# Optimization experiments

Hardware: AMD Instinct MI355X
Metric: run time of the kernel (lower is better)

Reference implementation:

```python
import jax, jax.numpy as jnp
import numpy as np

N_NODES = 50000
N_EDGES = 1600000
GL = [512, 256, 16]
LL = [16, 16]


def setup_inputs() -> dict:
    key = jax.random.key(0)
    ks = jax.random.split(key, 10)
    H = jax.random.normal(ks[0], (N_NODES, GL[0]), dtype=jnp.float32)
    edge_index = jax.random.randint(ks[1], (2, N_EDGES), 0, N_NODES, dtype=jnp.int64)
    edge_vals = jax.random.uniform(ks[2], (N_EDGES,), dtype=jnp.float32)
    def uni(k, shape, fan_out):
        stdv = 1.0 / np.sqrt(fan_out)
        return jax.random.uniform(k, shape, minval=-stdv, maxval=stdv, dtype=jnp.float32)
    W1 = uni(ks[3], (GL[0], GL[1]), GL[1])
    b1 = uni(ks[4], (GL[1],), GL[1])
    W2 = uni(ks[5], (GL[1], GL[2]), GL[2])
    b2 = uni(ks[6], (GL[2],), GL[2])
    Wl = uni(ks[7], (LL[0], LL[1]), LL[0])
    bl = uni(ks[8], (LL[1],), LL[0])
    return {"H": H, "edge_index": edge_index, "edge_vals": edge_vals,
            "W1": W1, "b1": b1, "W2": W2, "b2": b2, "Wl": Wl, "bl": bl}


def reference(H, edge_index, edge_vals, W1, b1, W2, b2, Wl, bl):
    row, col = edge_index[0], edge_index[1]
    n = H.shape[0]

    def spmm(X):  # (A @ X) for sparse COO A, X: [N, d]
        return jax.ops.segment_sum(edge_vals[:, None] * X[col], row, num_segments=n)

    # graph conv layers (dropout condition idx < len-2 never fires with 2 layers)
    H1 = jax.nn.relu(spmm(H @ W1) + b1)
    H2 = jax.nn.relu(spmm(H1 @ W2) + b2)
    # linear head
    H3 = jax.nn.relu(H2 @ Wl + bl)
    Y = jax.nn.softmax(H3, axis=1)  # [N, g]

    # NCut loss: sum_e w_e * dot(Y[row_e]/Gamma, (1-Y)[col_e])
    D = jax.ops.segment_sum(edge_vals, row, num_segments=n)  # degree [N]
    Gamma = Y.T @ D  # [g]
    YbyG = Y / Gamma[None, :]
    loss = jnp.sum(jnp.sum(YbyG[row] * (1.0 - Y)[col], axis=1) * edge_vals)
    return jnp.reshape(loss, (1,))
```

## Files before the change

kernel.cpp:

```cpp
#include <hip/hip_runtime.h>


constexpr int NN = 50000;
constexpr int NE = 1600000;
constexpr int F0 = 512;
constexpr int F1 = 256;
constexpr int G  = 16;
constexpr int CB   = 196;
constexpr int CCAP = 10240;
constexpr int CHUNK = 4096;
constexpr int NGEMM = 391 * 2;
constexpr int NPASS = 391;

typedef short  s16x8 __attribute__((ext_vector_type(8)));
typedef float  f32x4 __attribute__((ext_vector_type(4)));
typedef float  f32x2 __attribute__((ext_vector_type(2)));
typedef int    i32x4 __attribute__((ext_vector_type(4)));
typedef int    i32x2 __attribute__((ext_vector_type(2)));
typedef float  fv4   __attribute__((ext_vector_type(4)));

static __device__ __forceinline__ unsigned short f2bf(float f) {
    union { float f; unsigned u; } v; v.f = f;
    unsigned r = (v.u + 0x7FFFu + ((v.u >> 16) & 1u)) >> 16;
    return (unsigned short)r;
}
static __device__ __forceinline__ float bf2f(unsigned short u) {
    union { unsigned u; float f; } v; v.u = (unsigned)u << 16;
    return v.f;
}

__global__ __launch_bounds__(256) void k_castW1(const float* __restrict__ W1, unsigned short* __restrict__ W1t) {
    int idx = blockIdx.x * 256 + threadIdx.x;
    if (idx < F0 * F1) {
        int k = idx >> 8, n = idx & 255;
        W1t[n * F0 + k] = f2bf(W1[idx]);
    }
}

__global__ __launch_bounds__(256) void k_fused1(const float* __restrict__ H,
                                                const unsigned short* __restrict__ W1t,
                                                unsigned char* __restrict__ XW,
                                                const int* __restrict__ row, const int* __restrict__ col,
                                                const float* __restrict__ ev,
                                                int* __restrict__ ccur, int2* __restrict__ cbuf) {
    __shared__ __align__(16) unsigned char smem[2 * 128 * 72 * 2];
    const int bid = blockIdx.x;
    const int tid = threadIdx.x;
    const int stripe = bid / 3;
    const int pos = bid - stripe * 3;

    if (pos != 1) {
        const int gidx = stripe * 2 + (pos >> 1);
        unsigned short (*As)[72] = (unsigned short(*)[72])smem;
        unsigned short (*Bs)[72] = (unsigned short(*)[72])(smem + 128 * 72 * 2);
        const int lane = tid & 63;
        const int wave = tid >> 6;
        const int bm = (gidx >> 1) * 128;
        const int bn = (gidx & 1) * 128;
        const int m_off = (wave & 1) * 64;
        const int n_off = (wave >> 1) * 64;
        const int l15  = lane & 15;
        const int quad = lane >> 4;

        f32x4 acc[4][4];
#pragma unroll
        for (int i = 0; i < 4; ++i)
#pragma unroll
            for (int j = 0; j < 4; ++j) acc[i][j] = (f32x4)0.f;

        const int arow = tid >> 4;
        const int akq  = tid & 15;
        const int brow = tid >> 3;
        const int bkq  = tid & 7;

        float4 ar[8];
        uint4  br[4];

#define LOAD_TILE(K0)                                                              \
        do {                                                                       \
            _Pragma("unroll")                                                      \
            for (int p = 0; p < 8; ++p) {                                          \
                int gr = bm + p * 16 + arow;                                       \
                ar[p] = (gr < NN)                                                  \
                    ? *(const float4*)&H[(size_t)gr * F0 + (K0) + akq * 4]         \
                    : make_float4(0.f, 0.f, 0.f, 0.f);                             \
            }                                                                      \
            _Pragma("unroll")                                                      \
            for (int p = 0; p < 4; ++p)                                            \
                br[p] = *(const uint4*)&W1t[(size_t)(bn + p * 32 + brow) * F0 + (K0) + bkq * 8]; \
        } while (0)

        LOAD_TILE(0);
        for (int k0 = 0; k0 < F0; k0 += 64) {
#pragma unroll
            for (int p = 0; p < 8; ++p) {
                unsigned d0 = (unsigned)f2bf(ar[p].x) | ((unsigned)f2bf(ar[p].y) << 16);
                unsigned d1 = (unsigned)f2bf(ar[p].z) | ((unsigned)f2bf(ar[p].w) << 16);
                *(uint2*)&As[p * 16 + arow][akq * 4] = make_uint2(d0, d1);
            }
#pragma unroll
            for (int p = 0; p < 4; ++p)
                *(uint4*)&Bs[p * 32 + brow][bkq * 8] = br[p];
            __syncthreads();
            if (k0 + 64 < F0) LOAD_TILE(k0 + 64);
#pragma unroll
            for (int kk = 0; kk < 64; kk += 32) {
                s16x8 af[4], bfr[4];
#pragma unroll
                for (int mi = 0; mi < 4; ++mi)
                    af[mi] = *(const s16x8*)&As[m_off + mi * 16 + l15][kk + quad * 8];
#pragma unroll
                for (int ni = 0; ni < 4; ++ni)
                    bfr[ni] = *(const s16x8*)&Bs[n_off + ni * 16 + l15][kk + quad * 8];
#pragma unroll
                for (int mi = 0; mi < 4; ++mi)
#pragma unroll
                    for (int ni = 0; ni < 4; ++ni)
                        acc[mi][ni] = __builtin_amdgcn_mfma_f32_16x16x32_bf16(af[mi], bfr[ni], acc[mi][ni], 0, 0, 0);
            }
            __syncthreads();
        }
#undef LOAD_TILE
#pragma unroll
        for (int mi = 0; mi < 4; ++mi) {
            int r0 = bm + m_off + mi * 16 + quad * 4;
#pragma unroll
            for (int reg = 0; reg < 4; ++reg) {
                int gr = r0 + reg;
                if (gr < NN) {
                    unsigned char* orow = &XW[(size_t)gr * F1 + bn + n_off];
#pragma unroll
                    for (int ni = 0; ni < 4; ++ni) {
                        int pk = __builtin_amdgcn_cvt_pk_fp8_f32(acc[mi][ni][reg], 0.f, 0, false);
                        orow[ni * 16 + l15] = (unsigned char)(pk & 0xff);
                    }
                }
            }
        }
    } else {
        int* hcnt  = (int*)smem;
        int* hbase = hcnt + CB;
        for (int i = tid; i < CB; i += 256) hcnt[i] = 0;
        __syncthreads();

        const int base4 = stripe * (CHUNK / 4);
        int recx[16]; float recw[16]; int cb[16];
#pragma unroll
        for (int k = 0; k < 4; ++k) {
            int i4 = base4 + k * 256 + tid;
            bool ok = i4 < NE / 4;
            i32x4 r = ok ? __builtin_nontemporal_load(&((const i32x4*)row)[i4]) : (i32x4)0;
            i32x4 c = ok ? __builtin_nontemporal_load(&((const i32x4*)col)[i4]) : (i32x4)0;
            fv4   w = ok ? __builtin_nontemporal_load(&((const fv4*)ev)[i4])   : (fv4)0.f;
            int rr[4] = {r.x, r.y, r.z, r.w};
            int cc[4] = {c.x, c.y, c.z, c.w};
            float ww[4] = {w.x, w.y, w.z, w.w};
#pragma unroll
            for (int j = 0; j < 4; ++j) {
                int slot = k * 4 + j;
                if (ok) {
                    cb[slot] = rr[j] >> 8;
                    atomicAdd(&hcnt[cb[slot]], 1);
                } else {
                    cb[slot] = -1;
                }
                recx[slot] = (cc[j] << 16) | (rr[j] & 255);
                recw[slot] = ww[j];
            }
        }
        __syncthreads();
        for (int i = tid; i < CB; i += 256) {
            int cnt = hcnt[i];
            hbase[i] = (cnt > 0) ? atomicAdd(&ccur[i], cnt) : 0;
            hcnt[i] = 0;
        }
        __syncthreads();
#pragma unroll
        for (int slot = 0; slot < 16; ++slot) {
            if (cb[slot] >= 0) {
                int p = hbase[cb[slot]] + atomicAdd(&hcnt[cb[slot]], 1);
                cbuf[(size_t)cb[slot] * CCAP + p] = make_int2(recx[slot], __float_as_int(recw[slot]));
            }
        }
    }
}

__global__ __launch_bounds__(256) void k_passB(const int2* __restrict__ cbuf, const int* __restrict__ ccur,
                                               int* __restrict__ rowptr, int2* __restrict__ E) {
    __shared__ int cnt[256];
    __shared__ int scn[256];
    __shared__ int red[4];
    const int cbk = blockIdx.x;
    const int tid = threadIdx.x;
    cnt[tid] = 0;

    int b = 0;
    for (int i = tid; i < cbk; i += 256) b += ccur[i];
#pragma unroll
    for (int off = 1; off < 64; off <<= 1) b += __shfl_xor(b, off, 64);
    if ((tid & 63) == 0) red[tid >> 6] = b;
    __syncthreads();
    const int base = red[0] + red[1] + red[2] + red[3];

    const int total = ccur[cbk];
    const int2* src = cbuf + (size_t)cbk * CCAP;
    for (int i = tid; i < total; i += 256) atomicAdd(&cnt[src[i].x & 255], 1);
    __syncthreads();

    scn[tid] = cnt[tid];
    __syncthreads();
    for (int off = 1; off < 256; off <<= 1) {
        int t = (tid >= off) ? scn[tid - off] : 0;
        __syncthreads();
        scn[tid] += t;
        __syncthreads();
    }
    const int excl = scn[tid] - cnt[tid];
    const int r = (cbk << 8) + tid;
    if (r <= NN) rowptr[r] = base + excl;
    __syncthreads();
    cnt[tid] = base + excl;
    __syncthreads();
    for (int i = tid; i < total; i += 256) {
        int2 rec = src[i];
        int rl = rec.x & 255;
        int c  = (int)((unsigned)rec.x >> 16);
        int p = atomicAdd(&cnt[rl], 1);
        E[p] = make_int2(c << 8, rec.y);
    }
}

__global__ __launch_bounds__(256) void k_spmm1(const unsigned char* __restrict__ XW, const int* __restrict__ rowptr,
                                               const int2* __restrict__ E,
                                               const float* __restrict__ b1, const float* __restrict__ W2,
                                               unsigned short* __restrict__ Z, float* __restrict__ Dv) {
    __shared__ float W2T[G * F1];
    const int tid = threadIdx.x;
#pragma unroll
    for (int it = 0; it < 16; ++it)
        W2T[it * 256 + tid] = W2[tid * 16 + it];
    __syncthreads();
    const int lane = tid & 63;
    const int lane4 = lane * 4;
    const int n = blockIdx.x * 4 + (tid >> 6);
    const int s = __builtin_amdgcn_readfirstlane(rowptr[n]);
    const int e = __builtin_amdgcn_readfirstlane(rowptr[n + 1]);
    const i32x2* Ev = (const i32x2*)E;

    float4 acc = make_float4(0.f, 0.f, 0.f, 0.f);
    float wsum = 0.f;
    int i = s;
    for (; i + 8 <= e; i += 8) {
        int of[8]; float w[8];
#pragma unroll
        for (int k = 0; k < 8; ++k) {
            i32x2 ed = __builtin_nontemporal_load(&Ev[i + k]);
            of[k] = ed.x; w[k] = __int_as_float(ed.y);
        }
        unsigned gg[8];
#pragma unroll
        for (int k = 0; k < 8; ++k) gg[k] = *(const unsigned*)(XW + of[k] + lane4);
#pragma unroll
        for (int k = 0; k < 8; ++k) {
            f32x2 lo = __builtin_amdgcn_cvt_pk_f32_fp8(gg[k], false);
            f32x2 hi = __builtin_amdgcn_cvt_pk_f32_fp8(gg[k], true);
            acc.x = fmaf(w[k], lo.x, acc.x); acc.y = fmaf(w[k], lo.y, acc.y);
            acc.z = fmaf(w[k], hi.x, acc.z); acc.w = fmaf(w[k], hi.y, acc.w);
            wsum += w[k];
        }
    }
    for (; i < e; i += 4) {
        int of[4]; float w[4];
#pragma unroll
        for (int k = 0; k < 4; ++k) {
            int idx = i + k;
            bool ok = idx < e;
            i32x2 ed = Ev[ok ? idx : s];
            of[k] = ed.x; w[k] = ok ? __int_as_float(ed.y) : 0.f;
        }
        unsigned gg[4];
#pragma unroll
        for (int k = 0; k < 4; ++k) gg[k] = *(const unsigned*)(XW + of[k] + lane4);
#pragma unroll
        for (int k = 0; k < 4; ++k) {
            f32x2 lo = __builtin_amdgcn_cvt_pk_f32_fp8(gg[k], false);
            f32x2 hi = __builtin_amdgcn_cvt_pk_f32_fp8(gg[k], true);
            acc.x = fmaf(w[k], lo.x, acc.x); acc.y = fmaf(w[k], lo.y, acc.y);
            acc.z = fmaf(w[k], hi.x, acc.z); acc.w = fmaf(w[k], hi.y, acc.w);
            wsum += w[k];
        }
    }
    if (lane == 0) Dv[n] = wsum;

    float4 bb = *(const float4*)&b1[lane * 4];
    float4 h;
    h.x = fmaxf(acc.x + bb.x, 0.f);
    h.y = fmaxf(acc.y + bb.y, 0.f);
    h.z = fmaxf(acc.z + bb.z, 0.f);
    h.w = fmaxf(acc.w + bb.w, 0.f);

    float p[G];
#pragma unroll
    for (int j = 0; j < G; ++j) {
        float4 w4 = *(const float4*)&W2T[j * F1 + lane * 4];
        p[j] = h.x * w4.x + h.y * w4.y + h.z * w4.z + h.w * w4.w;
    }
#pragma unroll
    for (int off = 1; off < 64; off <<= 1) {
#pragma unroll
        for (int j = 0; j < G; ++j) p[j] += __shfl_xor(p[j], off, 64);
    }
    if (lane == 0) {
        unsigned zp[8];
#pragma unroll
        for (int j = 0; j < 8; ++j)
            zp[j] = (unsigned)f2bf(p[2 * j]) | ((unsigned)f2bf(p[2 * j + 1]) << 16);
        uint4* zo = (uint4*)&Z[n * G];
        zo[0] = make_uint4(zp[0], zp[1], zp[2], zp[3]);
        zo[1] = make_uint4(zp[4], zp[5], zp[6], zp[7]);
    }
}

__global__ __launch_bounds__(256) void k_head(const unsigned short* __restrict__ Zb, const int* __restrict__ rowptr,
                                              const int2* __restrict__ E,
                                              const float* __restrict__ b2, const float* __restrict__ Wl,
                                              const float* __restrict__ bl, const float* __restrict__ Dv,
                                              unsigned short* __restrict__ Yb, float* __restrict__ GammaP) {
    __shared__ float WlS[G * G];
    __shared__ float gsh[G];
    const int tid = threadIdx.x;
    if (tid < G * G) WlS[tid] = Wl[tid];
    if (tid < G) gsh[tid] = 0.f;
    __syncthreads();
    const int lane = tid & 63;
    const int g = lane >> 3;
    const int d = lane & 7;
    const int n = blockIdx.x * 4 + (tid >> 6);
    const int s = __builtin_amdgcn_readfirstlane(rowptr[n]);
    const int e = __builtin_amdgcn_readfirstlane(rowptr[n + 1]);
    const char* Zc = (const char*)Zb;
    const i32x2* Ev = (const i32x2*)E;

    float a0 = 0.f, a1 = 0.f;
    for (int base = s; base < e; base += 16) {
        int i0 = base + g;
        int i1 = base + 8 + g;
        i32x2 e0 = __builtin_nontemporal_load(&Ev[(i0 < e) ? i0 : s]);
        i32x2 e1 = __builtin_nontemporal_load(&Ev[(i1 < e) ? i1 : s]);
        float w0 = (i0 < e) ? __int_as_float(e0.y) : 0.f;
        float w1 = (i1 < e) ? __int_as_float(e1.y) : 0.f;
        unsigned z0 = *(const unsigned*)(Zc + (e0.x >> 3) + d * 4);
        unsigned z1 = *(const unsigned*)(Zc + (e1.x >> 3) + d * 4);
        a0 = fmaf(w0, bf2f((unsigned short)(z0 & 0xffff)), a0);
        a1 = fmaf(w0, bf2f((unsigned short)(z0 >> 16)), a1);
        a0 = fmaf(w1, bf2f((unsigned short)(z1 & 0xffff)), a0);
        a1 = fmaf(w1, bf2f((unsigned short)(z1 >> 16)), a1);
    }
    a0 += __shfl_xor(a0, 8, 64);  a1 += __shfl_xor(a1, 8, 64);
    a0 += __shfl_xor(a0, 16, 64); a1 += __shfl_xor(a1, 16, 64);
    a0 += __shfl_xor(a0, 32, 64); a1 += __shfl_xor(a1, 32, 64);

    const int j = lane & 15;
    float e0v = __shfl(a0, j >> 1, 64);
    float e1v = __shfl(a1, j >> 1, 64);
    float accj = (j & 1) ? e1v : e0v;

    float h2 = fmaxf(accj + b2[j], 0.f);
    float s3 = 0.f;
#pragma unroll
    for (int k = 0; k < G; ++k) s3 = fmaf(__shfl(h2, k, 64), WlS[k * G + j], s3);
    float h3 = fmaxf(s3 + bl[j], 0.f);
    float m = h3;
    m = fmaxf(m, __shfl_xor(m, 1, 64));
    m = fmaxf(m, __shfl_xor(m, 2, 64));
    m = fmaxf(m, __shfl_xor(m, 4, 64));
    m = fmaxf(m, __shfl_xor(m, 8, 64));
    float ex = __expf(h3 - m);
    float se = ex;
    se += __shfl_xor(se, 1, 64);
    se += __shfl_xor(se, 2, 64);
    se += __shfl_xor(se, 4, 64);
    se += __shfl_xor(se, 8, 64);
    float y = ex / se;
    if (lane < G) {
        Yb[n * G + j] = f2bf(y);
        atomicAdd(&gsh[j], y * Dv[n]);
    }
    __syncthreads();
    if (tid < G) atomicAdd(&GammaP[(blockIdx.x & 63) * G + tid], gsh[tid]);
}

__global__ __launch_bounds__(256) void k_loss(const unsigned short* __restrict__ Yb, const int* __restrict__ rowptr,
                                              const int2* __restrict__ E, float* __restrict__ SjP) {
    __shared__ float sjsh[G];
    const int tid = threadIdx.x;
    if (tid < G) sjsh[tid] = 0.f;
    __syncthreads();
    const int lane = tid & 63;
    const int g = lane >> 3;
    const int d = lane & 7;
    const int n = blockIdx.x * 4 + (tid >> 6);
    const int s = __builtin_amdgcn_readfirstlane(rowptr[n]);
    const int e = __builtin_amdgcn_readfirstlane(rowptr[n + 1]);
    const char* Yc = (const char*)Yb;
    const i32x2* Ev = (const i32x2*)E;

    unsigned yr = *(const unsigned*)(Yc + ((size_t)n << 5) + d * 4);
    float y0 = bf2f((unsigned short)(yr & 0xffff));
    float y1 = bf2f((unsigned short)(yr >> 16));

    float s0 = 0.f, s1 = 0.f;
    for (int base = s; base < e; base += 16) {
        int i0 = base + g;
        int i1 = base + 8 + g;
        i32x2 e0 = __builtin_nontemporal_load(&Ev[(i0 < e) ? i0 : s]);
        i32x2 e1 = __builtin_nontemporal_load(&Ev[(i1 < e) ? i1 : s]);
        float w0 = (i0 < e) ? __int_as_float(e0.y) : 0.f;
        float w1 = (i1 < e) ? __int_as_float(e1.y) : 0.f;
        unsigned z0 = *(const unsigned*)(Yc + (e0.x >> 3) + d * 4);
        unsigned z1 = *(const unsigned*)(Yc + (e1.x >> 3) + d * 4);
        s0 = fmaf(w0 * y0, bf2f((unsigned short)(z0 & 0xffff)), s0);
        s1 = fmaf(w0 * y1, bf2f((unsigned short)(z0 >> 16)), s1);
        s0 = fmaf(w1 * y0, bf2f((unsigned short)(z1 & 0xffff)), s0);
        s1 = fmaf(w1 * y1, bf2f((unsigned short)(z1 >> 16)), s1);
    }
    s0 += __shfl_xor(s0, 8, 64);  s1 += __shfl_xor(s1, 8, 64);
    s0 += __shfl_xor(s0, 16, 64); s1 += __shfl_xor(s1, 16, 64);
    s0 += __shfl_xor(s0, 32, 64); s1 += __shfl_xor(s1, 32, 64);
    if (lane < 8) {
        atomicAdd(&sjsh[2 * lane],     s0);
        atomicAdd(&sjsh[2 * lane + 1], s1);
    }
    __syncthreads();
    if (tid < G) atomicAdd(&SjP[(blockIdx.x & 63) * G + tid], sjsh[tid]);
}

__global__ void k_final(const float* __restrict__ GammaP, const float* __restrict__ SjP,
                        float* __restrict__ out) {
    const int tid = threadIdx.x;
    const int j = tid & 15;
    float gam = 0.f, sj = 0.f;
    for (int b = 0; b < 64; ++b) {
        gam += GammaP[b * G + j];
        sj  += SjP[b * G + j];
    }
    float v = sj / gam;
    v += __shfl_xor(v, 1, 64);
    v += __shfl_xor(v, 2, 64);
    v += __shfl_xor(v, 4, 64);
    v += __shfl_xor(v, 8, 64);
    if (tid == 0) out[0] = 16.0f - v;
}

static inline size_t alignup(size_t x) { return (x + 255) & ~(size_t)255; }

extern "C" void kernel_launch(void* const* d_in, const int* in_sizes, int n_in,
                              void* d_out, int out_size, void* d_ws, size_t ws_size,
                              hipStream_t stream) {
    const float* H  = (const float*)d_in[0];
    const int*   ei = (const int*)d_in[1];
    const float* ev = (const float*)d_in[2];
    const float* W1 = (const float*)d_in[3];
    const float* b1 = (const float*)d_in[4];
    const float* W2 = (const float*)d_in[5];
    const float* b2 = (const float*)d_in[6];
    const float* Wl = (const float*)d_in[7];
    const float* bl = (const float*)d_in[8];
    const int* row = ei;
    const int* col = ei + NE;

    char* base = (char*)d_ws;
    size_t off = 0;
    unsigned char*  XW  = (unsigned char*)(base + off);  off = alignup(off + (size_t)NN * F1);
    unsigned short* W1t = (unsigned short*)(base + off); off = alignup(off + (size_t)F0 * F1 * 2);
    unsigned short* Z   = (unsigned short*)(base + off); off = alignup(off + (size_t)NN * G * 2);
    unsigned short* Yb  = (unsigned short*)(base + off); off = alignup(off + (size_t)NN * G * 2);
    float* Dv     = (float*)(base + off); off = alignup(off + (size_t)NN * 4);
    size_t zoff = off;
    int*   ccur   = (int*)(base + off);   off += (size_t)CB * 4;
    float* GammaP = (float*)(base + off); off += (size_t)64 * G * 4;
    float* SjP    = (float*)(base + off); off += (size_t)64 * G * 4;
    size_t zsize = off - zoff;
    off = alignup(off);
    int*   rowptr = (int*)(base + off);   off = alignup(off + (size_t)(NN + 1) * 4);
    int2*  cbuf   = (int2*)(base + off);  off = alignup(off + (size_t)CB * CCAP * 8);
    int2*  E      = (int2*)(base + off);  off = alignup(off + (size_t)NE * 8);

    hipMemsetAsync(base + zoff, 0, zsize, stream);

    k_castW1<<<dim3((F0 * F1 + 255) / 256), dim3(256), 0, stream>>>(W1, W1t);
    k_fused1<<<dim3(3 * NPASS), dim3(256), 0, stream>>>(
        H, W1t, XW, row, col, ev, ccur, cbuf);
    k_passB<<<dim3(CB), dim3(256), 0, stream>>>(cbuf, ccur, rowptr, E);
    k_spmm1<<<dim3(NN / 4), dim3(256), 0, stream>>>(XW, rowptr, E, b1, W2, Z, Dv);
    k_head<<<dim3(NN / 4), dim3(256), 0, stream>>>(Z, rowptr, E, b2, Wl, bl, Dv, Yb, GammaP);
    k_loss<<<dim3(NN / 4), dim3(256), 0, stream>>>(Yb, rowptr, E, SjP);
    k_final<<<dim3(1), dim3(64), 0, stream>>>(GammaP, SjP, (float*)d_out);
}
```

Baseline: 403.7 us.

## Remap SpMM1 to 16 lanes per node with 16-byte gathers

Changes k_spmm1 from one 64-lane wavefront per node (4 bytes of fp8 per lane) to 16 lanes per node, each loading 16 bytes, so one block handles 16 nodes. This uses wider vector loads per gathered row, cuts the shuffle reduction from 6 to 4 steps and quarters the grid size. The cost is more registers per thread and more divergence, because the four nodes sharing a wavefront now have different edge counts. The 8-wide unrolled main loop is also removed, leaving only the 4-wide loop.

```diff
diff --git a/kernel.cpp b/kernel.cpp
--- a/kernel.cpp
+++ b/kernel.cpp
@@ -240,77 +240,75 @@
     for (int it = 0; it < 16; ++it)
         W2T[it * 256 + tid] = W2[tid * 16 + it];
     __syncthreads();
-    const int lane = tid & 63;
-    const int lane4 = lane * 4;
-    const int n = blockIdx.x * 4 + (tid >> 6);
-    const int s = __builtin_amdgcn_readfirstlane(rowptr[n]);
-    const int e = __builtin_amdgcn_readfirstlane(rowptr[n + 1]);
+    const int lane16 = tid & 15;
+    const int loff = lane16 * 16;
+    const int n = blockIdx.x * 16 + (tid >> 4);
+    const int s = rowptr[n];
+    const int e = rowptr[n + 1];
     const i32x2* Ev = (const i32x2*)E;
 
-    float4 acc = make_float4(0.f, 0.f, 0.f, 0.f);
+    float acc[16];
+#pragma unroll
+    for (int q = 0; q < 16; ++q) acc[q] = 0.f;
     float wsum = 0.f;
-    int i = s;
-    for (; i + 8 <= e; i += 8) {
-        int of[8]; float w[8];
-#pragma unroll
-        for (int k = 0; k < 8; ++k) {
-            i32x2 ed = __builtin_nontemporal_load(&Ev[i + k]);
-            of[k] = ed.x; w[k] = __int_as_float(ed.y);
-        }
-        unsigned gg[8];
-#pragma unroll
-        for (int k = 0; k < 8; ++k) gg[k] = *(const unsigned*)(XW + of[k] + lane4);
-#pragma unroll
-        for (int k = 0; k < 8; ++k) {
-            f32x2 lo = __builtin_amdgcn_cvt_pk_f32_fp8(gg[k], false);
-            f32x2 hi = __builtin_amdgcn_cvt_pk_f32_fp8(gg[k], true);
-            acc.x = fmaf(w[k], lo.x, acc.x); acc.y = fmaf(w[k], lo.y, acc.y);
-            acc.z = fmaf(w[k], hi.x, acc.z); acc.w = fmaf(w[k], hi.y, acc.w);
-            wsum += w[k];
-        }
-    }
-    for (; i < e; i += 4) {
+
+    for (int i = s; i < e; i += 4) {
         int of[4]; float w[4];
 #pragma unroll
         for (int k = 0; k < 4; ++k) {
             int idx = i + k;
             bool ok = idx < e;
-            i32x2 ed = Ev[ok ? idx : s];
+            i32x2 ed = __builtin_nontemporal_load(&Ev[ok ? idx : s]);
             of[k] = ed.x; w[k] = ok ? __int_as_float(ed.y) : 0.f;
         }
-        unsigned gg[4];
-#pragma unroll
-        for (int k = 0; k < 4; ++k) gg[k] = *(const unsigned*)(XW + of[k] + lane4);
+        uint4 gg[4];
+#pragma unroll
+        for (int k = 0; k < 4; ++k)
+            gg[k] = *(const uint4*)(XW + of[k] + loff);
 #pragma unroll
         for (int k = 0; k < 4; ++k) {
-            f32x2 lo = __builtin_amdgcn_cvt_pk_f32_fp8(gg[k], false);
-            f32x2 hi = __builtin_amdgcn_cvt_pk_f32_fp8(gg[k], true);
-            acc.x = fmaf(w[k], lo.x, acc.x); acc.y = fmaf(w[k], lo.y, acc.y);
-            acc.z = fmaf(w[k], hi.x, acc.z); acc.w = fmaf(w[k], hi.y, acc.w);
+            const unsigned gw[4] = {gg[k].x, gg[k].y, gg[k].z, gg[k].w};
+#pragma unroll
+            for (int q = 0; q < 4; ++q) {
+                f32x2 lo = __builtin_amdgcn_cvt_pk_f32_fp8(gw[q], false);
+                f32x2 hi = __builtin_amdgcn_cvt_pk_f32_fp8(gw[q], true);
+                acc[q * 4 + 0] = fmaf(w[k], lo.x, acc[q * 4 + 0]);
+                acc[q * 4 + 1] = fmaf(w[k], lo.y, acc[q * 4 + 1]);
+                acc[q * 4 + 2] = fmaf(w[k], hi.x, acc[q * 4 + 2]);
+                acc[q * 4 + 3] = fmaf(w[k], hi.y, acc[q * 4 + 3]);
+            }
             wsum += w[k];
         }
     }
-    if (lane == 0) Dv[n] = wsum;
-
-    float4 bb = *(const float4*)&b1[lane * 4];
-    float4 h;
-    h.x = fmaxf(acc.x + bb.x, 0.f);
-    h.y = fmaxf(acc.y + bb.y, 0.f);
-    h.z = fmaxf(acc.z + bb.z, 0.f);
-    h.w = fmaxf(acc.w + bb.w, 0.f);
+    if (lane16 == 0) Dv[n] = wsum;
+
+#pragma unroll
+    for (int q = 0; q < 4; ++q) {
+        float4 bb = *(const float4*)&b1[loff + q * 4];
+        acc[q * 4 + 0] = fmaxf(acc[q * 4 + 0] + bb.x, 0.f);
+        acc[q * 4 + 1] = fmaxf(acc[q * 4 + 1] + bb.y, 0.f);
+        acc[q * 4 + 2] = fmaxf(acc[q * 4 + 2] + bb.z, 0.f);
+        acc[q * 4 + 3] = fmaxf(acc[q * 4 + 3] + bb.w, 0.f);
+    }
 
     float p[G];
 #pragma unroll
     for (int j = 0; j < G; ++j) {
-        float4 w4 = *(const float4*)&W2T[j * F1 + lane * 4];
-        p[j] = h.x * w4.x + h.y * w4.y + h.z * w4.z + h.w * w4.w;
-    }
-#pragma unroll
-    for (int off = 1; off < 64; off <<= 1) {
+        float pj = 0.f;
+#pragma unroll
+        for (int q = 0; q < 4; ++q) {
+            float4 w4 = *(const float4*)&W2T[j * F1 + loff + q * 4];
+            pj += acc[q * 4 + 0] * w4.x + acc[q * 4 + 1] * w4.y
+                + acc[q * 4 + 2] * w4.z + acc[q * 4 + 3] * w4.w;
+        }
+        p[j] = pj;
+    }
+#pragma unroll
+    for (int off = 1; off < 16; off <<= 1) {
 #pragma unroll
         for (int j = 0; j < G; ++j) p[j] += __shfl_xor(p[j], off, 64);
     }
-    if (lane == 0) {
+    if (lane16 == 0) {
         unsigned zp[8];
 #pragma unroll
         for (int j = 0; j < 8; ++j)
@@ -492,7 +490,7 @@
     k_fused1<<<dim3(3 * NPASS), dim3(256), 0, stream>>>(
         H, W1t, XW, row, col, ev, ccur, cbuf);
     k_passB<<<dim3(CB), dim3(256), 0, stream>>>(cbuf, ccur, rowptr, E);
-    k_spmm1<<<dim3(NN / 4), dim3(256), 0, stream>>>(XW, rowptr, E, b1, W2, Z, Dv);
+    k_spmm1<<<dim3(NN / 16), dim3(256), 0, stream>>>(XW, rowptr, E, b1, W2, Z, Dv);
     k_head<<<dim3(NN / 4), dim3(256), 0, stream>>>(Z, rowptr, E, b2, Wl, bl, Dv, Yb, GammaP);
     k_loss<<<dim3(NN / 4), dim3(256), 0, stream>>>(Yb, rowptr, E, SjP);
     k_final<<<dim3(1), dim3(64), 0, stream>>>(GammaP, SjP, (float*)d_out);
```

Measured after the change: 397.5 us. No clear change (-1.5%).
